# Kernel tuning notes

Measured on AMD Instinct MI355X. Metric: run time of the kernel, lower is better.

The kernel has to match this reference:

```python
import jax, jax.numpy as jnp
import numpy as np

NUM_RELS = 64
EDGES_PER_REL = 16384
N_NODES = 100000
IN_FEAT = 128
OUT_FEAT = 128
NUM_BASES = 16
E = NUM_RELS * EDGES_PER_REL


def setup_inputs() -> dict:
    key = jax.random.key(0)
    ks = jax.random.split(key, 8)
    feat = jax.random.normal(ks[0], (N_NODES, IN_FEAT), dtype=jnp.float32)
    weight = jax.random.normal(ks[1], (NUM_BASES, IN_FEAT, OUT_FEAT), dtype=jnp.float32) * 0.05
    w_comp = jax.random.normal(ks[2], (NUM_RELS, NUM_BASES), dtype=jnp.float32) * 0.3
    h_bias = jnp.zeros((OUT_FEAT,), dtype=jnp.float32)
    loop_weight = jax.random.normal(ks[3], (IN_FEAT, OUT_FEAT), dtype=jnp.float32) * 0.05
    norm = jax.random.uniform(ks[4], (E, 1), dtype=jnp.float32)
    src = jax.random.randint(ks[5], (E,), 0, N_NODES, dtype=jnp.int32).astype(jnp.int64)
    dst = jax.random.randint(ks[6], (E,), 0, N_NODES, dtype=jnp.int32).astype(jnp.int64)
    # edges are sorted by relation type with uniform per-relation sections
    etypes = jnp.repeat(jnp.arange(NUM_RELS, dtype=jnp.int64), EDGES_PER_REL)
    return {"feat": feat, "weight": weight, "w_comp": w_comp, "h_bias": h_bias,
            "loop_weight": loop_weight, "norm": norm, "src": src, "dst": dst,
            "etypes": etypes, "section": EDGES_PER_REL}


def reference(feat, weight, w_comp, h_bias, loop_weight, norm, src, dst, etypes, section):
    num_rels, num_bases = w_comp.shape
    n_nodes, in_feat = feat.shape
    out_feat = weight.shape[2]
    # basis composition: per-relation weights [R, in, out]
    W = jnp.matmul(w_comp, weight.reshape(num_bases, in_feat * out_feat))
    W = W.reshape(num_rels, in_feat, out_feat)
    # gather per-edge source features (edges sorted by relation, uniform sections)
    h_e = feat[src]                                   # [E, in]
    n_edges = h_e.shape[0]
    h_r = h_e.reshape(num_rels, section, in_feat)     # [R, e_r, in]
    msg = jnp.einsum('rei,rio->reo', h_r, W)          # grouped matmul
    msg = msg.reshape(n_edges, out_feat) * norm       # edge-norm scaling
    # scatter-sum aggregation to destination nodes
    node_repr = jax.ops.segment_sum(msg, dst, num_segments=n_nodes)
    node_repr = node_repr + h_bias + jnp.matmul(feat, loop_weight)
    return jax.nn.relu(node_repr)
```

## Files before the change

kernel.cpp:

```cpp
#include <hip/hip_runtime.h>

#define N_NODES 100000
#define N_PAD 100352
#define NBLK 392
#define IN_FEAT 128
#define OUT_FEAT 128
#define NUM_RELS 64
#define EDGES_PER_REL 16384
#define NUM_BASES 16
#define E_TOTAL (NUM_RELS * EDGES_PER_REL)
#define TPB 4

typedef __bf16 bf16x8 __attribute__((ext_vector_type(8)));
typedef float floatx4 __attribute__((ext_vector_type(4)));

__global__ __launch_bounds__(256) void compose_all_bf16_kernel(
    const float* __restrict__ weight, const float* __restrict__ w_comp,
    const float* __restrict__ loop_w, __bf16* __restrict__ Wp,
    __bf16* __restrict__ Lp) {
  int gid = blockIdx.x * 256 + threadIdx.x;
  if (gid < NUM_RELS * 16384) {
    int r = gid >> 14;
    int off = gid & 16383;
    int j = off & 7, n = (off >> 3) & 127, kp = off >> 10;
    int k = kp * 8 + j;
    const float* wc = w_comp + r * NUM_BASES;
    float acc = 0.f;
#pragma unroll
    for (int b = 0; b < NUM_BASES; ++b)
      acc += wc[b] * weight[b * 16384 + k * 128 + n];
    Wp[gid] = (__bf16)acc;
  } else {
    int idx = gid - NUM_RELS * 16384;
    int j = idx & 7, n = (idx >> 3) & 127, kp = idx >> 10;
    Lp[idx] = (__bf16)loop_w[(kp * 8 + j) * 128 + n];
  }
}

__global__ __launch_bounds__(256) void compose_w_f32_kernel(
    const float* __restrict__ weight, const float* __restrict__ w_comp,
    float* __restrict__ W) {
  int idx = blockIdx.x * 256 + threadIdx.x;
  int r = idx >> 14;
  int io = idx & 16383;
  const float* wc = w_comp + r * NUM_BASES;
  float acc = 0.f;
#pragma unroll
  for (int b = 0; b < NUM_BASES; ++b)
    acc += wc[b] * weight[b * 16384 + io];
  W[idx] = acc;
}

__global__ __launch_bounds__(256) void init_out_mfma(
    const float* __restrict__ feat, __bf16* __restrict__ featb,
    const __bf16* __restrict__ Lp, const float* __restrict__ bias,
    float* __restrict__ out) {
  __shared__ __bf16 A_lds[64 * 136];
  int t = threadIdx.x;
  long base = (long)blockIdx.x * 64;
#pragma unroll
  for (int j = 0; j < 8; ++j) {
    int idx = t + j * 256;
    int e = idx >> 5, k4 = idx & 31;
    long n = base + e;
    float4 v = make_float4(0.f, 0.f, 0.f, 0.f);
    bool ok = (n < N_NODES);
    if (ok) v = ((const float4*)feat)[n * 32 + k4];
    __bf16 tb[4] = {(__bf16)v.x, (__bf16)v.y, (__bf16)v.z, (__bf16)v.w};
    *(ushort4*)&A_lds[e * 136 + k4 * 4] = *(ushort4*)tb;
    if (featb && ok)
      *(ushort4*)(featb + n * 128 + k4 * 4) = *(ushort4*)tb;
  }
  __syncthreads();

  int wave = t >> 6, lane = t & 63;
  int m16 = lane & 15, quad = lane >> 4;
  floatx4 acc[8];
#pragma unroll
  for (int nt = 0; nt < 8; ++nt) acc[nt] = (floatx4){0.f, 0.f, 0.f, 0.f};

  const __bf16* a_base = &A_lds[(wave * 16 + m16) * 136 + quad * 8];
#pragma unroll
  for (int ks = 0; ks < 4; ++ks) {
    bf16x8 a = *(const bf16x8*)(a_base + ks * 32);
    int kp = ks * 4 + quad;
#pragma unroll
    for (int nt = 0; nt < 8; ++nt) {
      bf16x8 b = *(const bf16x8*)(Lp + (kp * 128 + nt * 16 + m16) * 8);
      acc[nt] = __builtin_amdgcn_mfma_f32_16x16x32_bf16(a, b, acc[nt], 0, 0, 0);
    }
  }

  float bv[8];
#pragma unroll
  for (int nt = 0; nt < 8; ++nt) bv[nt] = bias[nt * 16 + m16];
#pragma unroll
  for (int r = 0; r < 4; ++r) {
    long n = base + wave * 16 + quad * 4 + r;
    if (n < N_NODES) {
#pragma unroll
      for (int nt = 0; nt < 8; ++nt)
        out[n * 128 + nt * 16 + m16] = acc[nt][r] + bv[nt];
    }
  }
}

__global__ __launch_bounds__(256) void zero_kernel(int* __restrict__ p) {
  p[blockIdx.x * 256 + threadIdx.x] = 0;
}

__global__ __launch_bounds__(256) void hist_rank_kernel(
    const int* __restrict__ dst, int* __restrict__ cnt8,
    int* __restrict__ rank, int cshift) {
  int e = blockIdx.x * 256 + threadIdx.x;
  int c = e >> cshift;
  rank[e] = atomicAdd(&cnt8[c * N_PAD + dst[e]], 1);
}

__global__ __launch_bounds__(256) void scan1_kernel(
    const int* __restrict__ cnt, int* __restrict__ row,
    int* __restrict__ bsum) {
  __shared__ int s[256];
  int t = threadIdx.x;
  int idx = blockIdx.x * 256 + t;
  int v = cnt[idx];
  s[t] = v;
  __syncthreads();
  for (int o = 1; o < 256; o <<= 1) {
    int x = (t >= o) ? s[t - o] : 0;
    __syncthreads();
    s[t] += x;
    __syncthreads();
  }
  row[idx] = s[t] - v;
  if (t == 255) bsum[blockIdx.x] = s[t];
}

__global__ __launch_bounds__(512) void scan2_kernel(
    const int* __restrict__ bsum, int* __restrict__ boff) {
  __shared__ int s[512];
  int t = threadIdx.x;
  int v = (t < NBLK) ? bsum[blockIdx.x * NBLK + t] : 0;
  s[t] = v;
  __syncthreads();
  for (int o = 1; o < 512; o <<= 1) {
    int x = (t >= o) ? s[t - o] : 0;
    __syncthreads();
    s[t] += x;
    __syncthreads();
  }
  if (t < NBLK) boff[blockIdx.x * NBLK + t] = s[t] - v;
}

__global__ __launch_bounds__(256) void scan3_kernel(
    int* __restrict__ row, const int* __restrict__ boff) {
  int idx = blockIdx.x * 256 + threadIdx.x;
  row[idx] += boff[blockIdx.x];
}

__global__ __launch_bounds__(256) void pos_fix_kernel(
    const int* __restrict__ dst, const int* __restrict__ row8,
    int* __restrict__ rank, int cshift) {
  int e = blockIdx.x * 256 + threadIdx.x;
  int c = e >> cshift;
  rank[e] += row8[(size_t)c * N_PAD + dst[e]];
}

__global__ __launch_bounds__(256) void edge_gemm_mfma(
    const float* __restrict__ feat, const __bf16* __restrict__ featb,
    const __bf16* __restrict__ Wp, const float* __restrict__ norm,
    const int* __restrict__ src, const int* __restrict__ pos,
    unsigned short* __restrict__ msg, int e_lo) {
  __shared__ __bf16 B_lds[IN_FEAT * OUT_FEAT];
  __shared__ __bf16 D_lds[4 * 4 * 136];
  int t = threadIdx.x;
  long base = (long)e_lo + (long)blockIdx.x * (64 * TPB);
  int rel = (int)(base >> 14);
  const __bf16* Wr = Wp + (long)rel * (IN_FEAT * OUT_FEAT);

  {
    const uint4* Wr4 = (const uint4*)Wr;
    uint4* B4 = (uint4*)B_lds;
#pragma unroll
    for (int j = 0; j < 8; ++j) B4[t + j * 256] = Wr4[t + j * 256];
  }

  int wave = t >> 6, lane = t & 63;
  int m16 = lane & 15, quad = lane >> 4;
  __bf16* Dw = &D_lds[wave * 544];

  bf16x8 aA[4], aB[4];
  float nmA[4], nmB[4];
  int poA[4], poB[4];
  int srow0, srow1;

#define LOAD_SROW(dstv, it) (dstv) = src[base + (it) * 64 + wave * 16 + m16]

#define LOAD_TILE(aX, nmX, poX, it, srowX)                                   \
  do {                                                                       \
    if (featb) {                                                             \
      const __bf16* ap = featb + (long)(srowX)*128 + quad * 8;               \
      _Pragma("unroll") for (int ks = 0; ks < 4; ++ks)                       \
          aX[ks] = *(const bf16x8*)(ap + ks * 32);                           \
    } else {                                                                 \
      const float* fp = feat + (long)(srowX)*128 + quad * 8;                 \
      _Pragma("unroll") for (int ks = 0; ks < 4; ++ks) {                     \
        float4 lo = *(const float4*)(fp + ks * 32);                          \
        float4 hi = *(const float4*)(fp + ks * 32 + 4);                      \
        __bf16 tb[8] = {(__bf16)lo.x, (__bf16)lo.y, (__bf16)lo.z,            \
                        (__bf16)lo.w, (__bf16)hi.x, (__bf16)hi.y,            \
                        (__bf16)hi.z, (__bf16)hi.w};                         \
        aX[ks] = *(bf16x8*)tb;                                               \
      }                                                                      \
    }                                                                        \
    _Pragma("unroll") for (int r = 0; r < 4; ++r) {                          \
      nmX[r] = norm[base + (it) * 64 + wave * 16 + quad * 4 + r];            \
      poX[r] = pos[base + (it) * 64 + wave * 16 + quad * 4 + r];             \
    }                                                                        \
  } while (0)

#define COMPUTE_TILE(aX, nmX, poX)                                           \
  do {                                                                       \
    floatx4 acc[8];                                                          \
    _Pragma("unroll") for (int nt = 0; nt < 8; ++nt)                         \
        acc[nt] = (floatx4){0.f, 0.f, 0.f, 0.f};                             \
    _Pragma("unroll") for (int ks = 0; ks < 4; ++ks) {                       \
      int kp = ks * 4 + quad;                                                \
      _Pragma("unroll") for (int nt = 0; nt < 8; ++nt) {                     \
        bf16x8 b = *(const bf16x8*)(B_lds + (kp * 128 + nt * 16 + m16) * 8); \
        acc[nt] =                                                            \
            __builtin_amdgcn_mfma_f32_16x16x32_bf16(aX[ks], b, acc[nt],      \
                                                    0, 0, 0);                \
      }                                                                      \
    }                                                                        \
           \
    _Pragma("unroll") for (int r = 0; r < 4; ++r) {                          \
      _Pragma("unroll") for (int nt = 0; nt < 8; ++nt)                       \
          Dw[quad * 136 + nt * 16 + m16] = (__bf16)(acc[nt][r] * nmX[r]);    \
      __builtin_amdgcn_wave_barrier();                                       \
      uint4 v = *(const uint4*)&Dw[quad * 136 + m16 * 8];                    \
      *(uint4*)(msg + (long)poX[r] * 128 + m16 * 8) = v;                     \
      __builtin_amdgcn_wave_barrier();                                       \
    }                                                                        \
  } while (0)

  LOAD_SROW(srow0, 0);
  LOAD_SROW(srow1, 1);
  LOAD_TILE(aA, nmA, poA, 0, srow0);
  __syncthreads();

  LOAD_TILE(aB, nmB, poB, 1, srow1);
  LOAD_SROW(srow0, 2);
  COMPUTE_TILE(aA, nmA, poA);

  LOAD_TILE(aA, nmA, poA, 2, srow0);
  LOAD_SROW(srow1, 3);
  COMPUTE_TILE(aB, nmB, poB);

  LOAD_TILE(aB, nmB, poB, 3, srow1);
  COMPUTE_TILE(aA, nmA, poA);

  COMPUTE_TILE(aB, nmB, poB);

#undef LOAD_SROW
#undef LOAD_TILE
#undef COMPUTE_TILE
}

__global__ __launch_bounds__(256) void gather_csr_kernel(
    const unsigned short* __restrict__ msg, const int* __restrict__ rowc,
    float* __restrict__ out, int do_relu) {
  int wave = threadIdx.x >> 6, lane = threadIdx.x & 63;
  int n = blockIdx.x * 4 + wave;
  if (n >= N_NODES) return;
  int beg = rowc[n], end = rowc[n + 1];
  if (!do_relu && beg == end) return;
  int q = lane >> 4;
  int c8 = lane & 15;
  float s[8] = {0.f, 0.f, 0.f, 0.f, 0.f, 0.f, 0.f, 0.f};
  for (int j = beg; j < end; j += 4) {
    int jr = j + q;
    if (jr < end) {
      uint4 m = *(const uint4*)(msg + (long)jr * 128 + c8 * 8);
      s[0] += __uint_as_float(m.x << 16);
      s[1] += __uint_as_float(m.x & 0xFFFF0000u);
      s[2] += __uint_as_float(m.y << 16);
      s[3] += __uint_as_float(m.y & 0xFFFF0000u);
      s[4] += __uint_as_float(m.z << 16);
      s[5] += __uint_as_float(m.z & 0xFFFF0000u);
      s[6] += __uint_as_float(m.w << 16);
      s[7] += __uint_as_float(m.w & 0xFFFF0000u);
    }
  }
#pragma unroll
  for (int k = 0; k < 8; ++k) {
    s[k] += __shfl_xor(s[k], 16);
    s[k] += __shfl_xor(s[k], 32);
  }
  if (q == 0) {
    float4 o0 = ((float4*)out)[(long)n * 32 + c8 * 2];
    float4 o1 = ((float4*)out)[(long)n * 32 + c8 * 2 + 1];
    o0.x += s[0]; o0.y += s[1]; o0.z += s[2]; o0.w += s[3];
    o1.x += s[4]; o1.y += s[5]; o1.z += s[6]; o1.w += s[7];
    if (do_relu) {
      o0.x = fmaxf(o0.x, 0.f); o0.y = fmaxf(o0.y, 0.f);
      o0.z = fmaxf(o0.z, 0.f); o0.w = fmaxf(o0.w, 0.f);
      o1.x = fmaxf(o1.x, 0.f); o1.y = fmaxf(o1.y, 0.f);
      o1.z = fmaxf(o1.z, 0.f); o1.w = fmaxf(o1.w, 0.f);
    }
    ((float4*)out)[(long)n * 32 + c8 * 2] = o0;
    ((float4*)out)[(long)n * 32 + c8 * 2 + 1] = o1;
  }
}

__global__ __launch_bounds__(256) void init_out_f32_kernel(
    const float* __restrict__ feat, const float* __restrict__ loop_w,
    const float* __restrict__ bias, float* __restrict__ out) {
  __shared__ float4 A4[64][32];
  int t = threadIdx.x;
  long base = (long)blockIdx.x * 64;
#pragma unroll
  for (int j = 0; j < 8; ++j) {
    int idx = t + j * 256;
    int e = idx >> 5, k4 = idx & 31;
    long n = base + e;
    float4 v = make_float4(0.f, 0.f, 0.f, 0.f);
    if (n < N_NODES) v = ((const float4*)feat)[n * 32 + k4];
    A4[e][k4] = v;
  }
  __syncthreads();
  int og = t & 31, eg = t >> 5;
  float acc[8][4];
#pragma unroll
  for (int j = 0; j < 8; ++j)
#pragma unroll
    for (int d = 0; d < 4; ++d) acc[j][d] = 0.f;
  const float4* W4 = (const float4*)loop_w;
  for (int k4 = 0; k4 < 32; ++k4) {
    float4 a[8];
#pragma unroll
    for (int j = 0; j < 8; ++j) a[j] = A4[eg * 8 + j][k4];
#pragma unroll
    for (int d = 0; d < 4; ++d) {
      float4 w = W4[(k4 * 4 + d) * 32 + og];
#pragma unroll
      for (int j = 0; j < 8; ++j) {
        float av = ((const float*)&a[j])[d];
        acc[j][0] += av * w.x;
        acc[j][1] += av * w.y;
        acc[j][2] += av * w.z;
        acc[j][3] += av * w.w;
      }
    }
  }
  float4 b = ((const float4*)bias)[og];
#pragma unroll
  for (int j = 0; j < 8; ++j) {
    long n = base + eg * 8 + j;
    if (n < N_NODES) {
      float4 v = make_float4(acc[j][0] + b.x, acc[j][1] + b.y,
                             acc[j][2] + b.z, acc[j][3] + b.w);
      ((float4*)out)[n * 32 + og] = v;
    }
  }
}

__global__ __launch_bounds__(256) void edge_msg_atomic_kernel(
    const float* __restrict__ feat, const float* __restrict__ W,
    const float* __restrict__ norm, const int* __restrict__ src,
    const int* __restrict__ dst, float* __restrict__ out) {
  __shared__ float4 A4[64][32];
  __shared__ int s_src[64];
  __shared__ int s_dst[64];
  __shared__ float s_norm[64];
  int t = threadIdx.x;
  long base = (long)blockIdx.x * 64;
  int rel = blockIdx.x >> 8;
  const float4* Wr4 = (const float4*)(W + (long)rel * IN_FEAT * OUT_FEAT);
  if (t < 64) {
    s_src[t] = src[base + t];
    s_dst[t] = dst[base + t];
    s_norm[t] = norm[base + t];
  }
  __syncthreads();
#pragma unroll
  for (int j = 0; j < 8; ++j) {
    int idx = t + j * 256;
    int e = idx >> 5, k4 = idx & 31;
    A4[e][k4] = ((const float4*)feat)[(long)s_src[e] * 32 + k4];
  }
  __syncthreads();
  int og = t & 31, eg = t >> 5;
  float acc[8][4];
#pragma unroll
  for (int j = 0; j < 8; ++j)
#pragma unroll
    for (int d = 0; d < 4; ++d) acc[j][d] = 0.f;
  for (int k4 = 0; k4 < 32; ++k4) {
    float4 a[8];
#pragma unroll
    for (int j = 0; j < 8; ++j) a[j] = A4[eg * 8 + j][k4];
#pragma unroll
    for (int d = 0; d < 4; ++d) {
      float4 w = Wr4[(k4 * 4 + d) * 32 + og];
#pragma unroll
      for (int j = 0; j < 8; ++j) {
        float av = ((const float*)&a[j])[d];
        acc[j][0] += av * w.x;
        acc[j][1] += av * w.y;
        acc[j][2] += av * w.z;
        acc[j][3] += av * w.w;
      }
    }
  }
#pragma unroll
  for (int j = 0; j < 8; ++j) {
    int e = eg * 8 + j;
    float nm = s_norm[e];
    float* orow = out + (long)s_dst[e] * OUT_FEAT + og * 4;
#pragma unroll
    for (int d = 0; d < 4; ++d) atomicAdd(orow + d, acc[j][d] * nm);
  }
}

__global__ __launch_bounds__(256) void relu_kernel(float* __restrict__ out) {
  int idx = blockIdx.x * 256 + threadIdx.x;
  float4 v = ((const float4*)out)[idx];
  v.x = fmaxf(v.x, 0.f);
  v.y = fmaxf(v.y, 0.f);
  v.z = fmaxf(v.z, 0.f);
  v.w = fmaxf(v.w, 0.f);
  ((float4*)out)[idx] = v;
}

extern "C" void kernel_launch(void* const* d_in, const int* in_sizes, int n_in,
                              void* d_out, int out_size, void* d_ws, size_t ws_size,
                              hipStream_t stream) {
  const float* feat   = (const float*)d_in[0];
  const float* weight = (const float*)d_in[1];
  const float* w_comp = (const float*)d_in[2];
  const float* h_bias = (const float*)d_in[3];
  const float* loop_w = (const float*)d_in[4];
  const float* norm   = (const float*)d_in[5];
  const int*   src    = (const int*)d_in[6];
  const int*   dst    = (const int*)d_in[7];
  float* out = (float*)d_out;

  const size_t SZ_WP   = (size_t)NUM_RELS * IN_FEAT * OUT_FEAT * 2;
  const size_t SZ_LP   = (size_t)IN_FEAT * OUT_FEAT * 2;
  const size_t SZ_FB   = (size_t)N_NODES * IN_FEAT * 2;
  const size_t SZ_RANK = (size_t)E_TOTAL * 4;

  int CH = 0, FB = 0;
  {
    const int chs[11] = {64, 64, 32, 32, 16, 16, 8, 8, 4, 4, 0};
    const int fbs[11] = { 1,  0,  1,  0,  1,  0, 1, 0, 1, 0, 0};
    for (int i = 0; i < 10 && CH == 0; ++i) {
      int ch = chs[i], fb = fbs[i], nc = NUM_RELS / ch;
      size_t need = SZ_WP + SZ_LP + (fb ? SZ_FB : 0) + SZ_RANK +
                    2 * (size_t)nc * N_PAD * 4 + 2 * (size_t)nc * NBLK * 4 +
                    (size_t)ch * EDGES_PER_REL * OUT_FEAT * 2;
      if (ws_size >= need) { CH = ch; FB = fb; }
    }
  }

  if (CH > 0) {
    const int NC = NUM_RELS / CH;
    const int chunk_edges = CH * EDGES_PER_REL;
    int cshift = 14;
    for (int x = CH; x > 1; x >>= 1) ++cshift;

    char* p = (char*)d_ws;
    __bf16* Wp = (__bf16*)p;                  p += SZ_WP;
    __bf16* Lp = (__bf16*)p;                  p += SZ_LP;
    __bf16* featb = nullptr;
    if (FB) { featb = (__bf16*)p;             p += SZ_FB; }
    int* rank = (int*)p;                      p += SZ_RANK;
    int* cnt8 = (int*)p;                      p += (size_t)NC * N_PAD * 4;
    int* row8 = (int*)p;                      p += (size_t)NC * N_PAD * 4;
    int* bsum = (int*)p;                      p += (size_t)NC * NBLK * 4;
    int* boff = (int*)p;                      p += (size_t)NC * NBLK * 4;
    unsigned short* msg = (unsigned short*)p;

    hipLaunchKernelGGL(compose_all_bf16_kernel,
                       dim3((NUM_RELS * 16384 + 16384) / 256), dim3(256), 0,
                       stream, weight, w_comp, loop_w, Wp, Lp);
    hipLaunchKernelGGL(init_out_mfma, dim3((N_NODES + 63) / 64), dim3(256), 0,
                       stream, feat, featb, Lp, h_bias, out);
    hipLaunchKernelGGL(zero_kernel, dim3(NC * NBLK), dim3(256), 0, stream, cnt8);
    hipLaunchKernelGGL(hist_rank_kernel, dim3(E_TOTAL / 256), dim3(256), 0,
                       stream, dst, cnt8, rank, cshift);
    hipLaunchKernelGGL(scan1_kernel, dim3(NC * NBLK), dim3(256), 0, stream,
                       cnt8, row8, bsum);
    hipLaunchKernelGGL(scan2_kernel, dim3(NC), dim3(512), 0, stream, bsum, boff);
    hipLaunchKernelGGL(scan3_kernel, dim3(NC * NBLK), dim3(256), 0, stream,
                       row8, boff);
    hipLaunchKernelGGL(pos_fix_kernel, dim3(E_TOTAL / 256), dim3(256), 0,
                       stream, dst, row8, rank, cshift);

    for (int c = 0; c < NC; ++c) {
      hipLaunchKernelGGL(edge_gemm_mfma, dim3(chunk_edges / (64 * TPB)),
                         dim3(256), 0, stream, feat, featb, Wp, norm, src,
                         rank, msg, c * chunk_edges);
      hipLaunchKernelGGL(gather_csr_kernel, dim3((N_NODES + 3) / 4), dim3(256),
                         0, stream, msg, row8 + (size_t)c * N_PAD, out,
                         (c == NC - 1) ? 1 : 0);
    }
  } else {
    float* W = (float*)d_ws;
    hipLaunchKernelGGL(init_out_f32_kernel, dim3((N_NODES + 63) / 64),
                       dim3(256), 0, stream, feat, loop_w, h_bias, out);
    hipLaunchKernelGGL(compose_w_f32_kernel, dim3(NUM_RELS * 16384 / 256),
                       dim3(256), 0, stream, weight, w_comp, W);
    hipLaunchKernelGGL(edge_msg_atomic_kernel, dim3(E_TOTAL / 64), dim3(256), 0,
                       stream, feat, W, norm, src, dst, out);
    hipLaunchKernelGGL(relu_kernel, dim3((N_NODES * OUT_FEAT / 4) / 256),
                       dim3(256), 0, stream, out);
  }
}
```

Before: 384.7 us.

## Move self-loop GEMM after aggregation and fold feat bf16 conversion into compose

The self-loop matmul, bias and ReLU now run in a final kernel that adds onto the aggregated output, and the first gather pass writes instead of read-modify-writing. The feat-to-bf16 conversion moves into the weight composition kernel, so one launch disappears and the first gather skips reading out. The final kernel reads its A operand straight from global memory rather than staging it in LDS, and it still has to read and rewrite out. The message staging buffer in LDS gets a larger row pitch, presumably to reduce bank conflicts.

After: 379.7 us. About the same (-1.3%).

```diff
diff --git a/kernel.cpp b/kernel.cpp
--- a/kernel.cpp
+++ b/kernel.cpp
@@ -10,16 +10,20 @@
 #define NUM_BASES 16
 #define E_TOTAL (NUM_RELS * EDGES_PER_REL)
 #define TPB 4
+#define W_WORK (NUM_RELS * 16384)
+#define L_WORK 16384
+#define F_WORK (N_NODES * IN_FEAT / 8)
 
 typedef __bf16 bf16x8 __attribute__((ext_vector_type(8)));
 typedef float floatx4 __attribute__((ext_vector_type(4)));
 
 __global__ __launch_bounds__(256) void compose_all_bf16_kernel(
     const float* __restrict__ weight, const float* __restrict__ w_comp,
-    const float* __restrict__ loop_w, __bf16* __restrict__ Wp,
-    __bf16* __restrict__ Lp) {
+    const float* __restrict__ loop_w, const float* __restrict__ feat,
+    __bf16* __restrict__ Wp, __bf16* __restrict__ Lp,
+    __bf16* __restrict__ featb) {
   int gid = blockIdx.x * 256 + threadIdx.x;
-  if (gid < NUM_RELS * 16384) {
+  if (gid < W_WORK) {
     int r = gid >> 14;
     int off = gid & 16383;
     int j = off & 7, n = (off >> 3) & 127, kp = off >> 10;
@@ -30,10 +34,18 @@
     for (int b = 0; b < NUM_BASES; ++b)
       acc += wc[b] * weight[b * 16384 + k * 128 + n];
     Wp[gid] = (__bf16)acc;
-  } else {
-    int idx = gid - NUM_RELS * 16384;
+  } else if (gid < W_WORK + L_WORK) {
+    int idx = gid - W_WORK;
     int j = idx & 7, n = (idx >> 3) & 127, kp = idx >> 10;
     Lp[idx] = (__bf16)loop_w[(kp * 8 + j) * 128 + n];
+  } else {
+    if (!featb) return;
+    long i = (long)(gid - W_WORK - L_WORK) * 8;
+    float4 a = *(const float4*)(feat + i);
+    float4 b = *(const float4*)(feat + i + 4);
+    __bf16 t8[8] = {(__bf16)a.x, (__bf16)a.y, (__bf16)a.z, (__bf16)a.w,
+                    (__bf16)b.x, (__bf16)b.y, (__bf16)b.z, (__bf16)b.w};
+    *(uint4*)(featb + i) = *(uint4*)t8;
   }
 }
 
@@ -51,43 +63,44 @@
   W[idx] = acc;
 }
 
-__global__ __launch_bounds__(256) void init_out_mfma(
-    const float* __restrict__ feat, __bf16* __restrict__ featb,
+__global__ __launch_bounds__(256) void finish_out_mfma(
+    const float* __restrict__ feat, const __bf16* __restrict__ featb,
     const __bf16* __restrict__ Lp, const float* __restrict__ bias,
     float* __restrict__ out) {
-  __shared__ __bf16 A_lds[64 * 136];
   int t = threadIdx.x;
   long base = (long)blockIdx.x * 64;
-#pragma unroll
-  for (int j = 0; j < 8; ++j) {
-    int idx = t + j * 256;
-    int e = idx >> 5, k4 = idx & 31;
-    long n = base + e;
-    float4 v = make_float4(0.f, 0.f, 0.f, 0.f);
-    bool ok = (n < N_NODES);
-    if (ok) v = ((const float4*)feat)[n * 32 + k4];
-    __bf16 tb[4] = {(__bf16)v.x, (__bf16)v.y, (__bf16)v.z, (__bf16)v.w};
-    *(ushort4*)&A_lds[e * 136 + k4 * 4] = *(ushort4*)tb;
-    if (featb && ok)
-      *(ushort4*)(featb + n * 128 + k4 * 4) = *(ushort4*)tb;
-  }
-  __syncthreads();
-
   int wave = t >> 6, lane = t & 63;
   int m16 = lane & 15, quad = lane >> 4;
+
+  long n_a = base + wave * 16 + m16;
+  long n_c = (n_a < N_NODES) ? n_a : (N_NODES - 1);
+  bf16x8 a[4];
+  if (featb) {
+    const __bf16* ap = featb + n_c * 128 + quad * 8;
+#pragma unroll
+    for (int ks = 0; ks < 4; ++ks) a[ks] = *(const bf16x8*)(ap + ks * 32);
+  } else {
+    const float* fp = feat + n_c * 128 + quad * 8;
+#pragma unroll
+    for (int ks = 0; ks < 4; ++ks) {
+      float4 lo = *(const float4*)(fp + ks * 32);
+      float4 hi = *(const float4*)(fp + ks * 32 + 4);
+      __bf16 tb[8] = {(__bf16)lo.x, (__bf16)lo.y, (__bf16)lo.z, (__bf16)lo.w,
+                      (__bf16)hi.x, (__bf16)hi.y, (__bf16)hi.z, (__bf16)hi.w};
+      a[ks] = *(bf16x8*)tb;
+    }
+  }
+
   floatx4 acc[8];
 #pragma unroll
   for (int nt = 0; nt < 8; ++nt) acc[nt] = (floatx4){0.f, 0.f, 0.f, 0.f};
-
-  const __bf16* a_base = &A_lds[(wave * 16 + m16) * 136 + quad * 8];
 #pragma unroll
   for (int ks = 0; ks < 4; ++ks) {
-    bf16x8 a = *(const bf16x8*)(a_base + ks * 32);
     int kp = ks * 4 + quad;
 #pragma unroll
     for (int nt = 0; nt < 8; ++nt) {
       bf16x8 b = *(const bf16x8*)(Lp + (kp * 128 + nt * 16 + m16) * 8);
-      acc[nt] = __builtin_amdgcn_mfma_f32_16x16x32_bf16(a, b, acc[nt], 0, 0, 0);
+      acc[nt] = __builtin_amdgcn_mfma_f32_16x16x32_bf16(a[ks], b, acc[nt], 0, 0, 0);
     }
   }
 
@@ -99,8 +112,10 @@
     long n = base + wave * 16 + quad * 4 + r;
     if (n < N_NODES) {
 #pragma unroll
-      for (int nt = 0; nt < 8; ++nt)
-        out[n * 128 + nt * 16 + m16] = acc[nt][r] + bv[nt];
+      for (int nt = 0; nt < 8; ++nt) {
+        float o = out[n * 128 + nt * 16 + m16] + acc[nt][r] + bv[nt];
+        out[n * 128 + nt * 16 + m16] = fmaxf(o, 0.f);
+      }
     }
   }
 }
@@ -172,7 +187,7 @@
     const int* __restrict__ src, const int* __restrict__ pos,
     unsigned short* __restrict__ msg, int e_lo) {
   __shared__ __bf16 B_lds[IN_FEAT * OUT_FEAT];
-  __shared__ __bf16 D_lds[4 * 4 * 136];
+  __shared__ __bf16 D_lds[4 * 4 * 144];
   int t = threadIdx.x;
   long base = (long)e_lo + (long)blockIdx.x * (64 * TPB);
   int rel = (int)(base >> 14);
@@ -187,7 +202,7 @@
 
   int wave = t >> 6, lane = t & 63;
   int m16 = lane & 15, quad = lane >> 4;
-  __bf16* Dw = &D_lds[wave * 544];
+  __bf16* Dw = &D_lds[wave * 576];
 
   bf16x8 aA[4], aB[4];
   float nmA[4], nmB[4];
@@ -236,9 +251,9 @@
            \
     _Pragma("unroll") for (int r = 0; r < 4; ++r) {                          \
       _Pragma("unroll") for (int nt = 0; nt < 8; ++nt)                       \
-          Dw[quad * 136 + nt * 16 + m16] = (__bf16)(acc[nt][r] * nmX[r]);    \
+          Dw[quad * 144 + nt * 16 + m16] = (__bf16)(acc[nt][r] * nmX[r]);    \
       __builtin_amdgcn_wave_barrier();                                       \
-      uint4 v = *(const uint4*)&Dw[quad * 136 + m16 * 8];                    \
+      uint4 v = *(const uint4*)&Dw[quad * 144 + m16 * 8];                    \
       *(uint4*)(msg + (long)poX[r] * 128 + m16 * 8) = v;                     \
       __builtin_amdgcn_wave_barrier();                                       \
     }                                                                        \
@@ -269,12 +284,12 @@
 
 __global__ __launch_bounds__(256) void gather_csr_kernel(
     const unsigned short* __restrict__ msg, const int* __restrict__ rowc,
-    float* __restrict__ out, int do_relu) {
+    float* __restrict__ out, int write_mode) {
   int wave = threadIdx.x >> 6, lane = threadIdx.x & 63;
   int n = blockIdx.x * 4 + wave;
   if (n >= N_NODES) return;
   int beg = rowc[n], end = rowc[n + 1];
-  if (!do_relu && beg == end) return;
+  if (!write_mode && beg == end) return;
   int q = lane >> 4;
   int c8 = lane & 15;
   float s[8] = {0.f, 0.f, 0.f, 0.f, 0.f, 0.f, 0.f, 0.f};
@@ -298,18 +313,19 @@
     s[k] += __shfl_xor(s[k], 32);
   }
   if (q == 0) {
-    float4 o0 = ((float4*)out)[(long)n * 32 + c8 * 2];
-    float4 o1 = ((float4*)out)[(long)n * 32 + c8 * 2 + 1];
-    o0.x += s[0]; o0.y += s[1]; o0.z += s[2]; o0.w += s[3];
-    o1.x += s[4]; o1.y += s[5]; o1.z += s[6]; o1.w += s[7];
-    if (do_relu) {
-      o0.x = fmaxf(o0.x, 0.f); o0.y = fmaxf(o0.y, 0.f);
-      o0.z = fmaxf(o0.z, 0.f); o0.w = fmaxf(o0.w, 0.f);
-      o1.x = fmaxf(o1.x, 0.f); o1.y = fmaxf(o1.y, 0.f);
-      o1.z = fmaxf(o1.z, 0.f); o1.w = fmaxf(o1.w, 0.f);
-    }
-    ((float4*)out)[(long)n * 32 + c8 * 2] = o0;
-    ((float4*)out)[(long)n * 32 + c8 * 2 + 1] = o1;
+    if (write_mode) {
+      ((float4*)out)[(long)n * 32 + c8 * 2] =
+          make_float4(s[0], s[1], s[2], s[3]);
+      ((float4*)out)[(long)n * 32 + c8 * 2 + 1] =
+          make_float4(s[4], s[5], s[6], s[7]);
+    } else {
+      float4 o0 = ((float4*)out)[(long)n * 32 + c8 * 2];
+      float4 o1 = ((float4*)out)[(long)n * 32 + c8 * 2 + 1];
+      o0.x += s[0]; o0.y += s[1]; o0.z += s[2]; o0.w += s[3];
+      o1.x += s[4]; o1.y += s[5]; o1.z += s[6]; o1.w += s[7];
+      ((float4*)out)[(long)n * 32 + c8 * 2] = o0;
+      ((float4*)out)[(long)n * 32 + c8 * 2 + 1] = o1;
+    }
   }
 }
 
@@ -483,10 +499,8 @@
     unsigned short* msg = (unsigned short*)p;
 
     hipLaunchKernelGGL(compose_all_bf16_kernel,
-                       dim3((NUM_RELS * 16384 + 16384) / 256), dim3(256), 0,
-                       stream, weight, w_comp, loop_w, Wp, Lp);
-    hipLaunchKernelGGL(init_out_mfma, dim3((N_NODES + 63) / 64), dim3(256), 0,
-                       stream, feat, featb, Lp, h_bias, out);
+                       dim3((W_WORK + L_WORK + F_WORK) / 256), dim3(256), 0,
+                       stream, weight, w_comp, loop_w, feat, Wp, Lp, featb);
     hipLaunchKernelGGL(zero_kernel, dim3(NC * NBLK), dim3(256), 0, stream, cnt8);
     hipLaunchKernelGGL(hist_rank_kernel, dim3(E_TOTAL / 256), dim3(256), 0,
                        stream, dst, cnt8, rank, cshift);
@@ -504,8 +518,10 @@
                          rank, msg, c * chunk_edges);
       hipLaunchKernelGGL(gather_csr_kernel, dim3((N_NODES + 3) / 4), dim3(256),
                          0, stream, msg, row8 + (size_t)c * N_PAD, out,
-                         (c == NC - 1) ? 1 : 0);
-    }
+                         (c == 0) ? 1 : 0);
+    }
+    hipLaunchKernelGGL(finish_out_mfma, dim3((N_NODES + 63) / 64), dim3(256),
+                       0, stream, feat, featb, Lp, h_bias, out);
   } else {
     float* W = (float*)d_ws;
     hipLaunchKernelGGL(init_out_f32_kernel, dim3((N_NODES + 63) / 64),
```
